# Optimization experiments

Hardware: AMD Instinct MI355X
Metric: run time of the kernel (lower is better)

## Reference

```python
import jax, jax.numpy as jnp
import numpy as np

F = 50          # num features
CARD = 10000    # cardinality per feature
D = 64          # factor_dim
A = 64          # attention_size
IU, JU = np.triu_indices(F, k=1)  # upper-triangular pair indices, P = F*(F-1)/2


def setup_inputs() -> dict:
    key = jax.random.key(0)
    ks = jax.random.split(key, 8)
    inputs = jax.random.randint(ks[0], (1024, F), 0, CARD, dtype=jnp.int32)
    emb_table = jax.random.normal(ks[1], (F * CARD, D), dtype=jnp.float32) * 0.05
    w_lin = jax.random.normal(ks[2], (F * CARD,), dtype=jnp.float32) * 0.05
    b_lin = jnp.zeros((1,), dtype=jnp.float32)
    W1 = jax.random.normal(ks[3], (D, A), dtype=jnp.float32) * (1.0 / np.sqrt(D))
    b1 = jnp.zeros((A,), dtype=jnp.float32)
    W2 = jax.random.normal(ks[4], (A, 1), dtype=jnp.float32) * (1.0 / np.sqrt(A))
    b2 = jnp.zeros((1,), dtype=jnp.float32)
    return {"inputs": inputs, "emb_table": emb_table, "w_lin": w_lin,
            "b_lin": b_lin, "W1": W1, "b1": b1, "W2": W2, "b2": b2}


def reference(inputs, emb_table, w_lin, b_lin, W1, b1, W2, b2):
    # Per-feature tables are stacked into one flat table; offset indices per feature.
    flat_idx = inputs + (jnp.arange(F, dtype=jnp.int32) * CARD)[None, :]  # [B, F]
    line_out = jnp.sum(w_lin[flat_idx], axis=1, keepdims=True) + b_lin    # [B, 1]
    factor = emb_table[flat_idx]                                          # [B, F, D]
    # Upper-triangular pairwise element-wise products (i < j), P = F(F-1)/2
    inter = factor[:, IU, :] * factor[:, JU, :]                           # [B, P, D]
    # Attention: Dense(A) -> ReLU -> Dense(1) -> Softmax over pairs
    h = jax.nn.relu(jnp.einsum('bpd,da->bpa', inter, W1) + b1)            # [B, P, A]
    logits = jnp.einsum('bpa,ao->bpo', h, W2) + b2                        # [B, P, 1]
    scores = jax.nn.softmax(logits, axis=1)                               # [B, P, 1]
    pooled = jnp.sum(inter, axis=-1, keepdims=True)                       # [B, P, 1]
    return line_out + jnp.sum(pooled * scores, axis=1)                    # [B, 1]
```

## Files before the change

### kernel.cpp

```cpp
#include <hip/hip_runtime.h>
#include <math.h>

#define FN 50
#define CARD 10000
#define NP 1225
#define NTILE 77
#define NPAD (NTILE*16)
#define FSTRIDE 72

typedef _Float16 half8 __attribute__((ext_vector_type(8)));
typedef __fp16 half2t __attribute__((ext_vector_type(2)));
typedef float floatx4 __attribute__((ext_vector_type(4)));

static __device__ __forceinline__ half2t h2max0(half2t v) {
  half2t r;
  r[0] = v[0] > (__fp16)0 ? v[0] : (__fp16)0;
  r[1] = v[1] > (__fp16)0 ? v[1] : (__fp16)0;
  return r;
}

static __device__ __forceinline__ float hdot2(half2t a, half2t b, float c) {
#if __has_builtin(__builtin_amdgcn_fdot2)
  return __builtin_amdgcn_fdot2(a, b, c, false);
#else
  return c + (float)a[0]*(float)b[0] + (float)a[1]*(float)b[1];
#endif
}

__global__ __launch_bounds__(256, 4)
void afm_kernel(const int* __restrict__ inp,
                const float* __restrict__ emb,
                const float* __restrict__ wlin,
                const float* __restrict__ blin,
                const float* __restrict__ W1,
                const float* __restrict__ b1,
                const float* __restrict__ W2,
                const float* __restrict__ b2,
                float* __restrict__ out)
{
  __shared__ __align__(16) _Float16 s_fac[FN][FSTRIDE];
  __shared__ unsigned int s_pij[NPAD];
  __shared__ float s_logit[NPAD], s_pool[NPAD];
  __shared__ float s_wl[FN];
  __shared__ float s_red[16];

  const int tid  = threadIdx.x;
  const int b    = blockIdx.x;
  const int lane = tid & 63;
  const int wave = tid >> 6;
  const int c    = lane & 15;
  const int kq   = lane >> 4;

  for (int p = tid; p < NPAD; p += 256) {
    int pp = p < NP ? p : NP - 1;
    int i = (int)((99.0f - sqrtf(9801.0f - 8.0f * (float)pp)) * 0.5f);
    if (i < 0) i = 0;
    while ((i + 1) * (98 - i) / 2 <= pp) ++i;
    while (i > 0 && i * (99 - i) / 2 > pp) --i;
    int j = pp - i * (99 - i) / 2 + i + 1;
    s_pij[p] = (unsigned)(i * (FSTRIDE * 2)) | ((unsigned)(j * (FSTRIDE * 2)) << 16);
  }

  const int* inprow = inp + b * FN;
  for (int idx = tid; idx < FN * 16; idx += 256) {
    int f = idx >> 4, q = idx & 15;
    long flat = (long)inprow[f] + f * CARD;
    floatx4 v = ((const floatx4*)emb)[flat * 16 + q];
    _Float16* dst = &s_fac[f][q * 4];
    dst[0] = (_Float16)v[0]; dst[1] = (_Float16)v[1];
    dst[2] = (_Float16)v[2]; dst[3] = (_Float16)v[3];
  }
  if (tid < FN) {
    int flat = inprow[tid] + tid * CARD;
    s_wl[tid] = wlin[flat];
  }

  half8 w1f[2][4];
#pragma unroll
  for (int ks = 0; ks < 2; ++ks)
#pragma unroll
    for (int mt = 0; mt < 4; ++mt)
#pragma unroll
      for (int jj = 0; jj < 4; ++jj) {
        float x = W1[(ks * 32 + kq * 8 + 2 * jj)     * 64 + mt * 16 + c];
        float y = W1[(ks * 32 + kq * 8 + 2 * jj + 1) * 64 + mt * 16 + c];
        half2t hw = __builtin_amdgcn_cvt_pkrtz(x, y);
        w1f[ks][mt][2 * jj]     = (_Float16)hw[0];
        w1f[ks][mt][2 * jj + 1] = (_Float16)hw[1];
      }
  half2t b1h[4][2], w2h[4][2];
#pragma unroll
  for (int mt = 0; mt < 4; ++mt) {
    floatx4 bv = ((const floatx4*)b1)[mt * 4 + kq];
    floatx4 wv = ((const floatx4*)W2)[mt * 4 + kq];
    b1h[mt][0] = __builtin_amdgcn_cvt_pkrtz(bv[0], bv[1]);
    b1h[mt][1] = __builtin_amdgcn_cvt_pkrtz(bv[2], bv[3]);
    w2h[mt][0] = __builtin_amdgcn_cvt_pkrtz(wv[0], wv[1]);
    w2h[mt][1] = __builtin_amdgcn_cvt_pkrtz(wv[2], wv[3]);
  }
  _Float16 onev = (c == 0) ? (_Float16)1 : (_Float16)0;
  half8 onesf = {onev, onev, onev, onev, onev, onev, onev, onev};

  __syncthreads();

  const char* fbase = (const char*)&s_fac[0][0];
  const int koff = kq * 16;
  for (int t = wave; t < NTILE; t += 4) {
    int p = t * 16 + c;
    unsigned po = s_pij[p];
    int offi = (int)(po & 0xffffu) + koff;
    int offj = (int)(po >> 16) + koff;
    half8 vi0 = *(const half8*)(fbase + offi);
    half8 vj0 = *(const half8*)(fbase + offj);
    half8 vi1 = *(const half8*)(fbase + offi + 64);
    half8 vj1 = *(const half8*)(fbase + offj + 64);
    half8 pr0 = vi0 * vj0;
    half8 pr1 = vi1 * vj1;
    floatx4 acc[5];
#pragma unroll
    for (int mt = 0; mt < 5; ++mt) acc[mt] = floatx4{0.f, 0.f, 0.f, 0.f};
#pragma unroll
    for (int mt = 0; mt < 4; ++mt) {
      acc[mt] = __builtin_amdgcn_mfma_f32_16x16x32_f16(w1f[0][mt], pr0, acc[mt], 0, 0, 0);
      acc[mt] = __builtin_amdgcn_mfma_f32_16x16x32_f16(w1f[1][mt], pr1, acc[mt], 0, 0, 0);
    }
    acc[4] = __builtin_amdgcn_mfma_f32_16x16x32_f16(onesf, pr0, acc[4], 0, 0, 0);
    acc[4] = __builtin_amdgcn_mfma_f32_16x16x32_f16(onesf, pr1, acc[4], 0, 0, 0);

    float lg = 0.f;
#pragma unroll
    for (int mt = 0; mt < 4; ++mt) {
      half2t h0 = __builtin_amdgcn_cvt_pkrtz(acc[mt][0], acc[mt][1]);
      half2t h1 = __builtin_amdgcn_cvt_pkrtz(acc[mt][2], acc[mt][3]);
      h0 = h2max0(h0 + b1h[mt][0]);
      h1 = h2max0(h1 + b1h[mt][1]);
      lg = hdot2(h0, w2h[mt][0], lg);
      lg = hdot2(h1, w2h[mt][1], lg);
    }
    lg += __shfl_xor(lg, 16, 64);
    lg += __shfl_xor(lg, 32, 64);
    if (lane < 16 && p < NP) {
      s_logit[p] = lg;
      s_pool[p]  = acc[4][0];
    }
  }

  __syncthreads();

  float m = -1e30f;
  for (int p = tid; p < NP; p += 256) m = fmaxf(m, s_logit[p]);
#pragma unroll
  for (int o = 32; o; o >>= 1) m = fmaxf(m, __shfl_xor(m, o, 64));
  if (lane == 0) s_red[wave] = m;
  __syncthreads();
  m = fmaxf(fmaxf(s_red[0], s_red[1]), fmaxf(s_red[2], s_red[3]));
  float se = 0.f, spe = 0.f;
  for (int p = tid; p < NP; p += 256) {
    float e = __expf(s_logit[p] - m);
    se += e;
    spe += e * s_pool[p];
  }
#pragma unroll
  for (int o = 32; o; o >>= 1) {
    se  += __shfl_xor(se, o, 64);
    spe += __shfl_xor(spe, o, 64);
  }
  if (lane == 0) { s_red[4 + wave] = se; s_red[8 + wave] = spe; }
  __syncthreads();
  if (tid == 0) {
    float line = blin[0];
#pragma unroll
    for (int f = 0; f < FN; ++f) line += s_wl[f];
    float SE  = s_red[4] + s_red[5] + s_red[6]  + s_red[7];
    float SPE = s_red[8] + s_red[9] + s_red[10] + s_red[11];
    out[b] = line + SPE / SE;
  }
}

extern "C" void kernel_launch(void* const* d_in, const int* in_sizes, int n_in,
                              void* d_out, int out_size, void* d_ws, size_t ws_size,
                              hipStream_t stream) {
  const int*   inp  = (const int*)d_in[0];
  const float* emb  = (const float*)d_in[1];
  const float* wlin = (const float*)d_in[2];
  const float* blin = (const float*)d_in[3];
  const float* W1   = (const float*)d_in[4];
  const float* b1   = (const float*)d_in[5];
  const float* W2   = (const float*)d_in[6];
  const float* b2   = (const float*)d_in[7];
  float* outp = (float*)d_out;
  const int B = in_sizes[0] / FN;
  afm_kernel<<<B, 256, 0, stream>>>(inp, emb, wlin, blin, W1, b1, W2, b2, outp);
}
```

Before: 26.56 us.

## Stage W1 fragments in LDS, fold bias into MFMA, prefetch next tile

W1 fragments are now built once per block into shared memory and read from LDS at each MFMA instead of being held in 32 VGPRs. The b1 bias is passed as the initial accumulator, which removes the separate half-precision bias add. The pair loop software-prefetches the next tile's factor vectors. The cross-lane shuffle reduction of logits is replaced by storing four fp16 partials per pair and summing them in the softmax pass. The aim is lower register pressure, higher occupancy and overlap of LDS latency with MFMA, at the cost of extra LDS traffic and fp16 partial rounding.

```diff
diff --git a/kernel.cpp b/kernel.cpp
--- a/kernel.cpp
+++ b/kernel.cpp
@@ -18,7 +18,6 @@
   r[1] = v[1] > (__fp16)0 ? v[1] : (__fp16)0;
   return r;
 }
-
 static __device__ __forceinline__ float hdot2(half2t a, half2t b, float c) {
 #if __has_builtin(__builtin_amdgcn_fdot2)
   return __builtin_amdgcn_fdot2(a, b, c, false);
@@ -39,8 +38,10 @@
                 float* __restrict__ out)
 {
   __shared__ __align__(16) _Float16 s_fac[FN][FSTRIDE];
-  __shared__ unsigned int s_pij[NPAD];
-  __shared__ float s_logit[NPAD], s_pool[NPAD];
+  __shared__ __align__(16) _Float16 s_w1[512 * 8];
+  __shared__ __align__(16) unsigned s_pij[NPAD];
+  __shared__ __align__(16) __fp16 s_lg4[NPAD * 4];
+  __shared__ float s_pool[NPAD];
   __shared__ float s_wl[FN];
   __shared__ float s_red[16];
 
@@ -64,8 +65,8 @@
   const int* inprow = inp + b * FN;
   for (int idx = tid; idx < FN * 16; idx += 256) {
     int f = idx >> 4, q = idx & 15;
-    long flat = (long)inprow[f] + f * CARD;
-    floatx4 v = ((const floatx4*)emb)[flat * 16 + q];
+    int flat = inprow[f] + f * CARD;
+    floatx4 v = ((const floatx4*)emb)[(long)flat * 16 + q];
     _Float16* dst = &s_fac[f][q * 4];
     dst[0] = (_Float16)v[0]; dst[1] = (_Float16)v[1];
     dst[2] = (_Float16)v[2]; dst[3] = (_Float16)v[3];
@@ -75,26 +76,22 @@
     s_wl[tid] = wlin[flat];
   }
 
-  half8 w1f[2][4];
-#pragma unroll
-  for (int ks = 0; ks < 2; ++ks)
-#pragma unroll
-    for (int mt = 0; mt < 4; ++mt)
-#pragma unroll
-      for (int jj = 0; jj < 4; ++jj) {
-        float x = W1[(ks * 32 + kq * 8 + 2 * jj)     * 64 + mt * 16 + c];
-        float y = W1[(ks * 32 + kq * 8 + 2 * jj + 1) * 64 + mt * 16 + c];
-        half2t hw = __builtin_amdgcn_cvt_pkrtz(x, y);
-        w1f[ks][mt][2 * jj]     = (_Float16)hw[0];
-        w1f[ks][mt][2 * jj + 1] = (_Float16)hw[1];
-      }
-  half2t b1h[4][2], w2h[4][2];
+  for (int ch = tid; ch < 512; ch += 256) {
+    int ks = ch >> 8, mt = (ch >> 6) & 3, ln = ch & 63;
+    int cc = ln & 15, kk = ln >> 4;
+    _Float16 tmp[8];
+#pragma unroll
+    for (int j = 0; j < 8; ++j)
+      tmp[j] = (_Float16)W1[(ks * 32 + kk * 8 + j) * 64 + mt * 16 + cc];
+    *(half8*)&s_w1[ch * 8] = *(const half8*)tmp;
+  }
+
+  floatx4 bias[4];
+  half2t w2h[4][2];
 #pragma unroll
   for (int mt = 0; mt < 4; ++mt) {
-    floatx4 bv = ((const floatx4*)b1)[mt * 4 + kq];
+    bias[mt] = ((const floatx4*)b1)[mt * 4 + kq];
     floatx4 wv = ((const floatx4*)W2)[mt * 4 + kq];
-    b1h[mt][0] = __builtin_amdgcn_cvt_pkrtz(bv[0], bv[1]);
-    b1h[mt][1] = __builtin_amdgcn_cvt_pkrtz(bv[2], bv[3]);
     w2h[mt][0] = __builtin_amdgcn_cvt_pkrtz(wv[0], wv[1]);
     w2h[mt][1] = __builtin_amdgcn_cvt_pkrtz(wv[2], wv[3]);
   }
@@ -103,52 +100,74 @@
 
   __syncthreads();
 
+#define LDW1(ks, mt) (*(const half8*)&s_w1[(((ks) * 4 + (mt)) * 64 + lane) * 8])
   const char* fbase = (const char*)&s_fac[0][0];
   const int koff = kq * 16;
-  for (int t = wave; t < NTILE; t += 4) {
-    int p = t * 16 + c;
-    unsigned po = s_pij[p];
-    int offi = (int)(po & 0xffffu) + koff;
-    int offj = (int)(po >> 16) + koff;
-    half8 vi0 = *(const half8*)(fbase + offi);
-    half8 vj0 = *(const half8*)(fbase + offj);
-    half8 vi1 = *(const half8*)(fbase + offi + 64);
-    half8 vj1 = *(const half8*)(fbase + offj + 64);
-    half8 pr0 = vi0 * vj0;
-    half8 pr1 = vi1 * vj1;
-    floatx4 acc[5];
-#pragma unroll
-    for (int mt = 0; mt < 5; ++mt) acc[mt] = floatx4{0.f, 0.f, 0.f, 0.f};
+
+  int t = wave;
+  int pcur = t * 16 + c;
+  unsigned po = s_pij[pcur];
+  int offi = (int)(po & 0xffffu) + koff;
+  int offj = (int)(po >> 16) + koff;
+  half8 cvi0 = *(const half8*)(fbase + offi);
+  half8 cvj0 = *(const half8*)(fbase + offj);
+  half8 cvi1 = *(const half8*)(fbase + offi + 64);
+  half8 cvj1 = *(const half8*)(fbase + offj + 64);
+
+  while (true) {
+    int tn = t + 4;
+    int pn = tn * 16 + c; if (pn > NPAD - 1) pn = NPAD - 1;
+    unsigned pon = s_pij[pn];
+
+    half8 pr0 = cvi0 * cvj0;
+    half8 pr1 = cvi1 * cvj1;
+
+    floatx4 acc[4];
 #pragma unroll
     for (int mt = 0; mt < 4; ++mt) {
-      acc[mt] = __builtin_amdgcn_mfma_f32_16x16x32_f16(w1f[0][mt], pr0, acc[mt], 0, 0, 0);
-      acc[mt] = __builtin_amdgcn_mfma_f32_16x16x32_f16(w1f[1][mt], pr1, acc[mt], 0, 0, 0);
+      acc[mt] = __builtin_amdgcn_mfma_f32_16x16x32_f16(LDW1(0, mt), pr0, bias[mt], 0, 0, 0);
+      acc[mt] = __builtin_amdgcn_mfma_f32_16x16x32_f16(LDW1(1, mt), pr1, acc[mt], 0, 0, 0);
     }
-    acc[4] = __builtin_amdgcn_mfma_f32_16x16x32_f16(onesf, pr0, acc[4], 0, 0, 0);
-    acc[4] = __builtin_amdgcn_mfma_f32_16x16x32_f16(onesf, pr1, acc[4], 0, 0, 0);
+    floatx4 accp = __builtin_amdgcn_mfma_f32_16x16x32_f16(onesf, pr0, (floatx4){0.f,0.f,0.f,0.f}, 0, 0, 0);
+    accp = __builtin_amdgcn_mfma_f32_16x16x32_f16(onesf, pr1, accp, 0, 0, 0);
+
+    int offi_n = (int)(pon & 0xffffu) + koff;
+    int offj_n = (int)(pon >> 16) + koff;
+    cvi0 = *(const half8*)(fbase + offi_n);
+    cvj0 = *(const half8*)(fbase + offj_n);
+    cvi1 = *(const half8*)(fbase + offi_n + 64);
+    cvj1 = *(const half8*)(fbase + offj_n + 64);
 
     float lg = 0.f;
 #pragma unroll
     for (int mt = 0; mt < 4; ++mt) {
       half2t h0 = __builtin_amdgcn_cvt_pkrtz(acc[mt][0], acc[mt][1]);
       half2t h1 = __builtin_amdgcn_cvt_pkrtz(acc[mt][2], acc[mt][3]);
-      h0 = h2max0(h0 + b1h[mt][0]);
-      h1 = h2max0(h1 + b1h[mt][1]);
+      h0 = h2max0(h0);
+      h1 = h2max0(h1);
       lg = hdot2(h0, w2h[mt][0], lg);
       lg = hdot2(h1, w2h[mt][1], lg);
     }
-    lg += __shfl_xor(lg, 16, 64);
-    lg += __shfl_xor(lg, 32, 64);
-    if (lane < 16 && p < NP) {
-      s_logit[p] = lg;
-      s_pool[p]  = acc[4][0];
-    }
-  }
-
-  __syncthreads();
-
+    s_lg4[pcur * 4 + kq] = (__fp16)lg;
+    if (kq == 0) s_pool[pcur] = accp[0];
+
+    t = tn;
+    if (t >= NTILE) break;
+    pcur = t * 16 + c;
+  }
+#undef LDW1
+
+  __syncthreads();
+
+  float* s_logit = (float*)s_pij;
   float m = -1e30f;
-  for (int p = tid; p < NP; p += 256) m = fmaxf(m, s_logit[p]);
+  for (int p = tid; p < NP; p += 256) {
+    const half2t* lp = (const half2t*)&s_lg4[p * 4];
+    half2t sfh = lp[0] + lp[1];
+    float lg = (float)sfh[0] + (float)sfh[1];
+    s_logit[p] = lg;
+    m = fmaxf(m, lg);
+  }
 #pragma unroll
   for (int o = 32; o; o >>= 1) m = fmaxf(m, __shfl_xor(m, o, 64));
   if (lane == 0) s_red[wave] = m;
```

New measurement: 24.81 us. -6.6%, faster.

## Tile pair computation by (i-row, 16-wide j-block) jobs with register reuse

Applied to the files above, without the earlier changes.

Each pair tile is now a fixed row i against a block of 16 consecutive j columns instead of 16 arbitrary linear pair indices. The i-factor is held in registers, the j-block is reloaded only when it changes, and the next job's i-factor is prefetched. W1 is transposed through LDS so the fragment loads are vectorised, b1 is folded into the MFMA accumulator init, and the cross-lane logit shuffles are replaced by per-kq fp16 partials summed in the softmax pass. The cost is some wasted MFMA work on masked lanes (146 jobs versus 77 dense tiles) and a little extra fp16 rounding of the partial logits.

```diff
diff --git a/kernel.cpp b/kernel.cpp
--- a/kernel.cpp
+++ b/kernel.cpp
@@ -4,8 +4,8 @@
 #define FN 50
 #define CARD 10000
 #define NP 1225
-#define NTILE 77
-#define NPAD (NTILE*16)
+#define NPAD 1232
+#define NJOBS 146
 #define FSTRIDE 72
 
 typedef _Float16 half8 __attribute__((ext_vector_type(8)));
@@ -18,7 +18,6 @@
   r[1] = v[1] > (__fp16)0 ? v[1] : (__fp16)0;
   return r;
 }
-
 static __device__ __forceinline__ float hdot2(half2t a, half2t b, float c) {
 #if __has_builtin(__builtin_amdgcn_fdot2)
   return __builtin_amdgcn_fdot2(a, b, c, false);
@@ -39,8 +38,11 @@
                 float* __restrict__ out)
 {
   __shared__ __align__(16) _Float16 s_fac[FN][FSTRIDE];
-  __shared__ unsigned int s_pij[NPAD];
-  __shared__ float s_logit[NPAD], s_pool[NPAD];
+  __shared__ __align__(16) _Float16 s_w1t[64][64];
+  __shared__ unsigned s_jobs[NJOBS + 2];
+  __shared__ __align__(8) __fp16 s_lg4[NPAD * 4];
+  __shared__ float s_pool[NPAD];
+  __shared__ float s_logit[NPAD];
   __shared__ float s_wl[FN];
   __shared__ float s_red[16];
 
@@ -51,21 +53,25 @@
   const int c    = lane & 15;
   const int kq   = lane >> 4;
 
-  for (int p = tid; p < NPAD; p += 256) {
-    int pp = p < NP ? p : NP - 1;
-    int i = (int)((99.0f - sqrtf(9801.0f - 8.0f * (float)pp)) * 0.5f);
-    if (i < 0) i = 0;
-    while ((i + 1) * (98 - i) / 2 <= pp) ++i;
-    while (i > 0 && i * (99 - i) / 2 > pp) --i;
-    int j = pp - i * (99 - i) / 2 + i + 1;
-    s_pij[p] = (unsigned)(i * (FSTRIDE * 2)) | ((unsigned)(j * (FSTRIDE * 2)) << 16);
+  if (tid < NJOBS) {
+    int t = tid;
+    int I, J, ii;
+    if (t < 144) {
+      int tp = t >> 4; ii = t & 15;
+      I = (tp < 4) ? 0 : (tp < 7) ? 1 : 2;
+      J = (tp < 4) ? tp : (tp < 7) ? (tp - 3) : (tp - 5);
+    } else { I = 3; J = 3; ii = t - 144; }
+    int i  = I * 16 + ii;
+    int jb = J * 16;
+    int pb1 = i * (99 - i) / 2 - i - 1 + jb + 1;
+    s_jobs[t] = (unsigned)i | ((unsigned)jb << 6) | ((unsigned)pb1 << 16);
   }
 
   const int* inprow = inp + b * FN;
   for (int idx = tid; idx < FN * 16; idx += 256) {
     int f = idx >> 4, q = idx & 15;
-    long flat = (long)inprow[f] + f * CARD;
-    floatx4 v = ((const floatx4*)emb)[flat * 16 + q];
+    int flat = inprow[f] + f * CARD;
+    floatx4 v = ((const floatx4*)emb)[(long)flat * 16 + q];
     _Float16* dst = &s_fac[f][q * 4];
     dst[0] = (_Float16)v[0]; dst[1] = (_Float16)v[1];
     dst[2] = (_Float16)v[2]; dst[3] = (_Float16)v[3];
@@ -75,26 +81,24 @@
     s_wl[tid] = wlin[flat];
   }
 
-  half8 w1f[2][4];
-#pragma unroll
-  for (int ks = 0; ks < 2; ++ks)
-#pragma unroll
-    for (int mt = 0; mt < 4; ++mt)
-#pragma unroll
-      for (int jj = 0; jj < 4; ++jj) {
-        float x = W1[(ks * 32 + kq * 8 + 2 * jj)     * 64 + mt * 16 + c];
-        float y = W1[(ks * 32 + kq * 8 + 2 * jj + 1) * 64 + mt * 16 + c];
-        half2t hw = __builtin_amdgcn_cvt_pkrtz(x, y);
-        w1f[ks][mt][2 * jj]     = (_Float16)hw[0];
-        w1f[ks][mt][2 * jj + 1] = (_Float16)hw[1];
-      }
-  half2t b1h[4][2], w2h[4][2];
+  {
+    int d = tid >> 2, a0 = (tid & 3) * 16;
+#pragma unroll
+    for (int r = 0; r < 4; ++r) {
+      floatx4 v = *(const floatx4*)&W1[d * 64 + a0 + r * 4];
+      s_w1t[a0 + r * 4 + 0][d] = (_Float16)v[0];
+      s_w1t[a0 + r * 4 + 1][d] = (_Float16)v[1];
+      s_w1t[a0 + r * 4 + 2][d] = (_Float16)v[2];
+      s_w1t[a0 + r * 4 + 3][d] = (_Float16)v[3];
+    }
+  }
+
+  floatx4 bias[4];
+  half2t w2h[4][2];
 #pragma unroll
   for (int mt = 0; mt < 4; ++mt) {
-    floatx4 bv = ((const floatx4*)b1)[mt * 4 + kq];
+    bias[mt] = ((const floatx4*)b1)[mt * 4 + kq];
     floatx4 wv = ((const floatx4*)W2)[mt * 4 + kq];
-    b1h[mt][0] = __builtin_amdgcn_cvt_pkrtz(bv[0], bv[1]);
-    b1h[mt][1] = __builtin_amdgcn_cvt_pkrtz(bv[2], bv[3]);
     w2h[mt][0] = __builtin_amdgcn_cvt_pkrtz(wv[0], wv[1]);
     w2h[mt][1] = __builtin_amdgcn_cvt_pkrtz(wv[2], wv[3]);
   }
@@ -103,52 +107,84 @@
 
   __syncthreads();
 
+  half8 w1f[2][4];
+#pragma unroll
+  for (int ks = 0; ks < 2; ++ks)
+#pragma unroll
+    for (int mt = 0; mt < 4; ++mt)
+      w1f[ks][mt] = *(const half8*)&s_w1t[mt * 16 + c][ks * 32 + kq * 8];
+
   const char* fbase = (const char*)&s_fac[0][0];
   const int koff = kq * 16;
-  for (int t = wave; t < NTILE; t += 4) {
-    int p = t * 16 + c;
-    unsigned po = s_pij[p];
-    int offi = (int)(po & 0xffffu) + koff;
-    int offj = (int)(po >> 16) + koff;
-    half8 vi0 = *(const half8*)(fbase + offi);
-    half8 vj0 = *(const half8*)(fbase + offj);
-    half8 vi1 = *(const half8*)(fbase + offi + 64);
-    half8 vj1 = *(const half8*)(fbase + offj + 64);
-    half8 pr0 = vi0 * vj0;
-    half8 pr1 = vi1 * vj1;
-    floatx4 acc[5];
-#pragma unroll
-    for (int mt = 0; mt < 5; ++mt) acc[mt] = floatx4{0.f, 0.f, 0.f, 0.f};
+  const floatx4 zf4 = {0.f, 0.f, 0.f, 0.f};
+
+  int jt = wave;
+  unsigned jw = s_jobs[jt];
+  int ci = jw & 63, cjb = (int)((jw >> 6) & 63), cpb = (int)(jw >> 16) - 1;
+  const char* fip = fbase + ci * (FSTRIDE * 2) + koff;
+  half8 fi0 = *(const half8*)(fip);
+  half8 fi1 = *(const half8*)(fip + 64);
+  int prevJb = -1;
+  half8 fj0, fj1;
+
+  while (true) {
+    if (cjb != prevJb) {
+      int jrow = cjb + c; if (jrow > FN - 1) jrow = FN - 1;
+      const char* fjp = fbase + jrow * (FSTRIDE * 2) + koff;
+      fj0 = *(const half8*)(fjp);
+      fj1 = *(const half8*)(fjp + 64);
+      prevJb = cjb;
+    }
+    int jn = jt + 4; if (jn > NJOBS - 1) jn = NJOBS - 1;
+    unsigned jwn = s_jobs[jn];
+    int ni = jwn & 63, njb = (int)((jwn >> 6) & 63), npb = (int)(jwn >> 16) - 1;
+    const char* fnp = fbase + ni * (FSTRIDE * 2) + koff;
+    half8 fin0 = *(const half8*)(fnp);
+    half8 fin1 = *(const half8*)(fnp + 64);
+
+    half8 pr0 = fi0 * fj0;
+    half8 pr1 = fi1 * fj1;
+
+    floatx4 acc[4];
+#pragma unroll
+    for (int mt = 0; mt < 4; ++mt)
+      acc[mt] = __builtin_amdgcn_mfma_f32_16x16x32_f16(w1f[0][mt], pr0, bias[mt], 0, 0, 0);
+#pragma unroll
+    for (int mt = 0; mt < 4; ++mt)
+      acc[mt] = __builtin_amdgcn_mfma_f32_16x16x32_f16(w1f[1][mt], pr1, acc[mt], 0, 0, 0);
+    floatx4 ap = __builtin_amdgcn_mfma_f32_16x16x32_f16(onesf, pr0, zf4, 0, 0, 0);
+    ap = __builtin_amdgcn_mfma_f32_16x16x32_f16(onesf, pr1, ap, 0, 0, 0);
+
+    float lg = 0.f;
 #pragma unroll
     for (int mt = 0; mt < 4; ++mt) {
-      acc[mt] = __builtin_amdgcn_mfma_f32_16x16x32_f16(w1f[0][mt], pr0, acc[mt], 0, 0, 0);
-      acc[mt] = __builtin_amdgcn_mfma_f32_16x16x32_f16(w1f[1][mt], pr1, acc[mt], 0, 0, 0);
-    }
-    acc[4] = __builtin_amdgcn_mfma_f32_16x16x32_f16(onesf, pr0, acc[4], 0, 0, 0);
-    acc[4] = __builtin_amdgcn_mfma_f32_16x16x32_f16(onesf, pr1, acc[4], 0, 0, 0);
-
-    float lg = 0.f;
-#pragma unroll
-    for (int mt = 0; mt < 4; ++mt) {
-      half2t h0 = __builtin_amdgcn_cvt_pkrtz(acc[mt][0], acc[mt][1]);
-      half2t h1 = __builtin_amdgcn_cvt_pkrtz(acc[mt][2], acc[mt][3]);
-      h0 = h2max0(h0 + b1h[mt][0]);
-      h1 = h2max0(h1 + b1h[mt][1]);
+      half2t h0 = h2max0(__builtin_amdgcn_cvt_pkrtz(acc[mt][0], acc[mt][1]));
+      half2t h1 = h2max0(__builtin_amdgcn_cvt_pkrtz(acc[mt][2], acc[mt][3]));
       lg = hdot2(h0, w2h[mt][0], lg);
       lg = hdot2(h1, w2h[mt][1], lg);
     }
-    lg += __shfl_xor(lg, 16, 64);
-    lg += __shfl_xor(lg, 32, 64);
-    if (lane < 16 && p < NP) {
-      s_logit[p] = lg;
-      s_pool[p]  = acc[4][0];
-    }
+
+    int j = cjb + c;
+    bool valid = (j > ci) && (j < FN);
+    if (valid) s_lg4[(cpb + c) * 4 + kq] = (__fp16)lg;
+    if (valid && kq == 0) s_pool[cpb + c] = ap[0];
+
+    jt += 4;
+    if (jt >= NJOBS) break;
+    ci = ni; cjb = njb; cpb = npb;
+    fi0 = fin0; fi1 = fin1;
   }
 
   __syncthreads();
 
   float m = -1e30f;
-  for (int p = tid; p < NP; p += 256) m = fmaxf(m, s_logit[p]);
+  for (int p = tid; p < NP; p += 256) {
+    const half2t* lp = (const half2t*)&s_lg4[p * 4];
+    half2t sfh = lp[0] + lp[1];
+    float lg = (float)sfh[0] + (float)sfh[1];
+    s_logit[p] = lg;
+    m = fmaxf(m, lg);
+  }
 #pragma unroll
   for (int o = 32; o; o >>= 1) m = fmaxf(m, __shfl_xor(m, o, 64));
   if (lane == 0) s_red[wave] = m;
```

New measurement: 35.17 us. +32.4%, slower.
